# Kernel tuning notes

Hardware: AMD Instinct MI355X
Metric: run time of the kernel (lower is better)

## Reference

```python
import jax, jax.numpy as jnp
from jax import lax
import numpy as np

N_ASSETS = 128
BATCH = 2048
MAX_WEIGHT = 1.0
N_ITERS = 300      # projected-gradient iterations (unrolled solver)
N_BISECT = 40      # bisection steps for simplex-box projection
LR = 0.02
EPS = 1e-8


def project_capped_simplex(v, c):
    """Project rows of v onto {w : sum(w)=1, -c <= w <= c} via bisection on the
    shift tau in w = clip(v - tau, -c, c). sum is decreasing in tau."""
    lo = jnp.min(v, axis=-1, keepdims=True) - c - 1.0
    hi = jnp.max(v, axis=-1, keepdims=True) + c

    def body(carry, _):
        lo, hi = carry
        mid = 0.5 * (lo + hi)
        s = jnp.sum(jnp.clip(v - mid, -c, c), axis=-1, keepdims=True)
        too_big = s > 1.0
        return (jnp.where(too_big, mid, lo), jnp.where(too_big, hi, mid)), None

    (lo, hi), _ = lax.scan(body, (lo, hi), None, length=N_BISECT)
    tau = 0.5 * (lo + hi)
    return jnp.clip(v - tau, -c, c)


def solve_markowitz(rets, A, alpha_abs, max_weight):
    """maximize r.w - sqrt(w'Aw) - alpha*||w||_2  s.t. sum w = 1, |w| <= c,
    via projected gradient ascent (fixed iteration count, fully batched)."""
    B, n = rets.shape
    w0 = jnp.full((B, n), 1.0 / n, dtype=rets.dtype)
    a = alpha_abs[:, None]

    def step(w, _):
        Aw = jnp.einsum('bij,bj->bi', A, w)                       # (B,n)
        risk = jnp.sqrt(jnp.sum(w * Aw, axis=-1, keepdims=True) + EPS)
        nrm = jnp.sqrt(jnp.sum(w * w, axis=-1, keepdims=True) + EPS)
        g = rets - Aw / risk - a * (w / nrm)                      # gradient of objective
        w_new = project_capped_simplex(w + LR * g, max_weight)
        return w_new, None

    w, _ = lax.scan(step, w0, None, length=N_ITERS)
    return w


def setup_inputs() -> dict:
    key = jax.random.key(0)
    k1, k2, k3, k4 = jax.random.split(key, 4)
    rets = 0.05 * jax.random.normal(k1, (BATCH, N_ASSETS), dtype=jnp.float32)
    # PSD covariance: B B^T / n + jitter*I
    Bm = jax.random.normal(k2, (BATCH, N_ASSETS, N_ASSETS), dtype=jnp.float32)
    covmat = jnp.einsum('bik,bjk->bij', Bm, Bm) / N_ASSETS
    covmat = covmat + 1e-3 * jnp.eye(N_ASSETS, dtype=jnp.float32)
    gamma = jax.random.uniform(k3, (BATCH,), dtype=jnp.float32, minval=0.1, maxval=2.0)
    alpha = jax.random.normal(k4, (BATCH,), dtype=jnp.float32)
    return {"rets": rets, "covmat": covmat, "gamma": gamma, "alpha": alpha}


def reference(rets, covmat, gamma, alpha):
    alpha_abs = jnp.abs(alpha)
    A = gamma[:, None, None] * covmat   # gamma-adjusted covariance, as in forward
    return solve_markowitz(rets, A, alpha_abs, MAX_WEIGHT)
```

## Files before the change

### kernel.cpp

```cpp
#include <hip/hip_runtime.h>
#include <math.h>

#define NA      128
#define NBATCH  2048
#define NTHR    512
#define NIT     300
#define NBIS    40
#define LRC     0.02f
#define EPSC    1e-8f

template <int CTRL>
__device__ __forceinline__ float dpp_sum_step(float x) {
  int s = __builtin_amdgcn_update_dpp(0, __float_as_int(x), CTRL, 0xF, 0xF, true);
  return x + __int_as_float(s);
}
__device__ __forceinline__ float wave_sum64(float x) {
  x = dpp_sum_step<0x111>(x);
  x = dpp_sum_step<0x112>(x);
  x = dpp_sum_step<0x114>(x);
  x = dpp_sum_step<0x118>(x);
  x = dpp_sum_step<0x142>(x);
  x = dpp_sum_step<0x143>(x);
  return x;
}
template <int CTRL>
__device__ __forceinline__ float dpp_mov_self(float x) {
  int s = __builtin_amdgcn_update_dpp(__float_as_int(x), __float_as_int(x), CTRL, 0xF, 0xF, false);
  return __int_as_float(s);
}
__device__ __forceinline__ float wave_min64(float x) {
  x = fminf(x, dpp_mov_self<0x111>(x));
  x = fminf(x, dpp_mov_self<0x112>(x));
  x = fminf(x, dpp_mov_self<0x114>(x));
  x = fminf(x, dpp_mov_self<0x118>(x));
  x = fminf(x, dpp_mov_self<0x142>(x));
  x = fminf(x, dpp_mov_self<0x143>(x));
  return x;
}
__device__ __forceinline__ float wave_max64(float x) {
  x = fmaxf(x, dpp_mov_self<0x111>(x));
  x = fmaxf(x, dpp_mov_self<0x112>(x));
  x = fmaxf(x, dpp_mov_self<0x114>(x));
  x = fmaxf(x, dpp_mov_self<0x118>(x));
  x = fmaxf(x, dpp_mov_self<0x142>(x));
  x = fmaxf(x, dpp_mov_self<0x143>(x));
  return x;
}
__device__ __forceinline__ float bcast63(float x) {
  return __int_as_float(__builtin_amdgcn_readlane(__float_as_int(x), 63));
}
__device__ __forceinline__ float clip1(float x) {
  return __builtin_amdgcn_fmed3f(x, -1.0f, 1.0f);
}

__global__ __launch_bounds__(NTHR)
void markowitz_kernel(
    const float* __restrict__ rets,
    const float* __restrict__ covmat,
    const float* __restrict__ gamma,
    const float* __restrict__ alpha,
    float* __restrict__ out)
{
  const int b    = blockIdx.x;
  const int tid  = threadIdx.x;
  const int r    = tid & (NA - 1);
  const int q    = tid >> 7;
  const int lane = tid & 63;
  const int wv   = tid >> 6;
  const int chain_wv = b & 7;

  __shared__ __align__(16) float ws[NA];
  __shared__ __align__(16) float vs[NA];
  __shared__ __align__(16) float part[NTHR];
  __shared__ float pp[4];

  const float gm = gamma[b];
  const float4* Aq = reinterpret_cast<const float4*>(
      covmat + (size_t)b * NA * NA + (size_t)r * NA + (size_t)q * 32);
  float4 a[8];
#pragma unroll
  for (int k = 0; k < 8; ++k) {
    float4 t = Aq[k];
    a[k] = make_float4(t.x * gm, t.y * gm, t.z * gm, t.w * gm);
  }
  const float av = fabsf(alpha[b]);
  float r_c = 0.0f;
  if (tid < NA) { r_c = rets[b * NA + tid]; ws[tid] = 1.0f / NA; }
  __syncthreads();

#pragma unroll 1
  for (int it = 0; it < NIT; ++it) {
    const float4* w4 = reinterpret_cast<const float4*>(ws) + q * 8;
    float4 acc = make_float4(0.f, 0.f, 0.f, 0.f);
#pragma unroll
    for (int k = 0; k < 8; ++k) {
      float4 wk = w4[k];
      acc.x = fmaf(a[k].x, wk.x, acc.x);
      acc.y = fmaf(a[k].y, wk.y, acc.y);
      acc.z = fmaf(a[k].z, wk.z, acc.z);
      acc.w = fmaf(a[k].w, wk.w, acc.w);
    }
    part[tid] = (acc.x + acc.y) + (acc.z + acc.w);
    __syncthreads();

    float Aw = 0.f, w_c = 0.f, v_c = 0.f;
    if (tid < NA) {
      Aw  = (part[tid] + part[tid + NA]) + (part[tid + 2 * NA] + part[tid + 3 * NA]);
      w_c = ws[tid];
      float p1 = wave_sum64(w_c * Aw);
      float p2 = wave_sum64(w_c * w_c);
      if (lane == 63) { pp[wv * 2 + 0] = p1; pp[wv * 2 + 1] = p2; }
    }
    __syncthreads();

    if (tid < NA) {
      const float risk = sqrtf(pp[0] + pp[2] + EPSC);
      const float nrm  = sqrtf(pp[1] + pp[3] + EPSC);
      const float g    = r_c - Aw / risk - av * (w_c / nrm);
      v_c = w_c + LRC * g;
      vs[tid] = v_c;
    }
    __syncthreads();

    if (wv == chain_wv) {
      float v0 = vs[lane];
      float v1 = vs[lane + 64];
      float mn = bcast63(wave_min64(fminf(v0, v1)));
      float mx = bcast63(wave_max64(fmaxf(v0, v1)));
      float lo = mn - 2.0f;
      float hi = mx + 1.0f;
#pragma unroll 1
      for (int rr = 0; rr < NBIS; ++rr) {
        const float mid = 0.5f * (lo + hi);
        float s = wave_sum64(clip1(v0 - mid) + clip1(v1 - mid));
        const float st = bcast63(s);
        const bool big = st > 1.0f;
        lo = big ? mid : lo;
        hi = big ? hi : mid;
      }
      const float tau = 0.5f * (lo + hi);
      ws[lane]      = clip1(v0 - tau);
      ws[lane + 64] = clip1(v1 - tau);
    }
    __syncthreads();
  }

  if (tid < NA) out[b * NA + tid] = ws[tid];
}

extern "C" void kernel_launch(void* const* d_in, const int* in_sizes, int n_in,
                              void* d_out, int out_size, void* d_ws, size_t ws_size,
                              hipStream_t stream) {
  const float* rets   = (const float*)d_in[0];
  const float* covmat = (const float*)d_in[1];
  const float* gamma  = (const float*)d_in[2];
  const float* alpha  = (const float*)d_in[3];
  float* out = (float*)d_out;

  hipLaunchKernelGGL(markowitz_kernel, dim3(NBATCH), dim3(NTHR), 0, stream,
                     rets, covmat, gamma, alpha, out);
}
```

Before: 2.691 ms.

## Halve block size and stream covariance from memory each iteration instead of registers

Each block now runs 256 threads instead of 512, and every thread handles two 32-column segments of its covariance row. The gamma-scaled covariance is no longer held in registers for the whole solve; it is reloaded from global memory on every one of the 300 iterations and scaled by gamma inline. The aim is lower register pressure and higher occupancy, and the wave that runs the bisection is chosen with a different hash of the block index. The cost is about 64KB of covariance traffic per block per iteration, which likely exceeds cache capacity across all blocks and may make the kernel memory-bound.

Measured after the change: 3.261 ms. +21.1%, slower.

```diff
diff --git a/kernel.cpp b/kernel.cpp
--- a/kernel.cpp
+++ b/kernel.cpp
@@ -3,7 +3,7 @@
 
 #define NA      128
 #define NBATCH  2048
-#define NTHR    512
+#define NTHR    256
 #define NIT     300
 #define NBIS    40
 #define LRC     0.02f
@@ -64,25 +64,20 @@
   const int b    = blockIdx.x;
   const int tid  = threadIdx.x;
   const int r    = tid & (NA - 1);
-  const int q    = tid >> 7;
+  const int q0   = tid >> 7;
   const int lane = tid & 63;
   const int wv   = tid >> 6;
-  const int chain_wv = b & 7;
+  const int chain_wv = ((b >> 8) ^ b) & 3;
 
   __shared__ __align__(16) float ws[NA];
   __shared__ __align__(16) float vs[NA];
-  __shared__ __align__(16) float part[NTHR];
+  __shared__ __align__(16) float part[4 * NA];
   __shared__ float pp[4];
 
   const float gm = gamma[b];
-  const float4* Aq = reinterpret_cast<const float4*>(
-      covmat + (size_t)b * NA * NA + (size_t)r * NA + (size_t)q * 32);
-  float4 a[8];
-#pragma unroll
-  for (int k = 0; k < 8; ++k) {
-    float4 t = Aq[k];
-    a[k] = make_float4(t.x * gm, t.y * gm, t.z * gm, t.w * gm);
-  }
+  const float* Arow = covmat + (size_t)b * NA * NA + (size_t)r * NA + (size_t)q0 * 32;
+  const float4* Aq0 = reinterpret_cast<const float4*>(Arow);
+  const float4* Aq1 = reinterpret_cast<const float4*>(Arow + 64);
   const float av = fabsf(alpha[b]);
   float r_c = 0.0f;
   if (tid < NA) { r_c = rets[b * NA + tid]; ws[tid] = 1.0f / NA; }
@@ -90,20 +85,30 @@
 
 #pragma unroll 1
   for (int it = 0; it < NIT; ++it) {
-    const float4* w4 = reinterpret_cast<const float4*>(ws) + q * 8;
-    float4 acc = make_float4(0.f, 0.f, 0.f, 0.f);
+    const float4* w40 = reinterpret_cast<const float4*>(ws) + q0 * 8;
+    const float4* w41 = w40 + 16;
+    float4 acc0 = make_float4(0.f, 0.f, 0.f, 0.f);
+    float4 acc1 = make_float4(0.f, 0.f, 0.f, 0.f);
 #pragma unroll
     for (int k = 0; k < 8; ++k) {
-      float4 wk = w4[k];
-      acc.x = fmaf(a[k].x, wk.x, acc.x);
-      acc.y = fmaf(a[k].y, wk.y, acc.y);
-      acc.z = fmaf(a[k].z, wk.z, acc.z);
-      acc.w = fmaf(a[k].w, wk.w, acc.w);
+      float4 t0 = Aq0[k];
+      float4 wk0 = w40[k];
+      acc0.x = fmaf(t0.x * gm, wk0.x, acc0.x);
+      acc0.y = fmaf(t0.y * gm, wk0.y, acc0.y);
+      acc0.z = fmaf(t0.z * gm, wk0.z, acc0.z);
+      acc0.w = fmaf(t0.w * gm, wk0.w, acc0.w);
+      float4 t1 = Aq1[k];
+      float4 wk1 = w41[k];
+      acc1.x = fmaf(t1.x * gm, wk1.x, acc1.x);
+      acc1.y = fmaf(t1.y * gm, wk1.y, acc1.y);
+      acc1.z = fmaf(t1.z * gm, wk1.z, acc1.z);
+      acc1.w = fmaf(t1.w * gm, wk1.w, acc1.w);
     }
-    part[tid] = (acc.x + acc.y) + (acc.z + acc.w);
+    part[tid]       = (acc0.x + acc0.y) + (acc0.z + acc0.w);
+    part[tid + 256] = (acc1.x + acc1.y) + (acc1.z + acc1.w);
     __syncthreads();
 
-    float Aw = 0.f, w_c = 0.f, v_c = 0.f;
+    float Aw = 0.f, w_c = 0.f;
     if (tid < NA) {
       Aw  = (part[tid] + part[tid + NA]) + (part[tid + 2 * NA] + part[tid + 3 * NA]);
       w_c = ws[tid];
@@ -117,8 +122,7 @@
       const float risk = sqrtf(pp[0] + pp[2] + EPSC);
       const float nrm  = sqrtf(pp[1] + pp[3] + EPSC);
       const float g    = r_c - Aw / risk - av * (w_c / nrm);
-      v_c = w_c + LRC * g;
-      vs[tid] = v_c;
+      vs[tid] = w_c + LRC * g;
     }
     __syncthreads();
 
```

## Map one wave per batch element and batch bisection across eight elements

Applied to the files above, without the earlier changes.

Each block now handles eight batch elements, one wave apiece. Each lane computes two rows of A·w by streaming the covariance rows from global memory every iteration, instead of holding a register-resident slice of A. That removes the cross-wave partial-sum exchange and two barriers per iteration. The bisection for all eight elements runs in a single wave, using 8-lane groups and DPP/swizzle reductions, with eight values per lane. The trade-off is re-reading 64KB of A per element every iteration through cache, plus fewer blocks overall.

New measurement: 3.227 ms. 1.2x slower.

```diff
diff --git a/kernel.cpp b/kernel.cpp
--- a/kernel.cpp
+++ b/kernel.cpp
@@ -4,10 +4,12 @@
 #define NA      128
 #define NBATCH  2048
 #define NTHR    512
+#define NELB    8
 #define NIT     300
 #define NBIS    40
 #define LRC     0.02f
 #define EPSC    1e-8f
+
 
 template <int CTRL>
 __device__ __forceinline__ float dpp_sum_step(float x) {
@@ -23,31 +25,17 @@
   x = dpp_sum_step<0x143>(x);
   return x;
 }
+__device__ __forceinline__ float bcast63(float x) {
+  return __int_as_float(__builtin_amdgcn_readlane(__float_as_int(x), 63));
+}
 template <int CTRL>
-__device__ __forceinline__ float dpp_mov_self(float x) {
-  int s = __builtin_amdgcn_update_dpp(__float_as_int(x), __float_as_int(x), CTRL, 0xF, 0xF, false);
+__device__ __forceinline__ float dpp_qp(float x) {
+  int s = __builtin_amdgcn_update_dpp(0, __float_as_int(x), CTRL, 0xF, 0xF, true);
   return __int_as_float(s);
 }
-__device__ __forceinline__ float wave_min64(float x) {
-  x = fminf(x, dpp_mov_self<0x111>(x));
-  x = fminf(x, dpp_mov_self<0x112>(x));
-  x = fminf(x, dpp_mov_self<0x114>(x));
-  x = fminf(x, dpp_mov_self<0x118>(x));
-  x = fminf(x, dpp_mov_self<0x142>(x));
-  x = fminf(x, dpp_mov_self<0x143>(x));
-  return x;
-}
-__device__ __forceinline__ float wave_max64(float x) {
-  x = fmaxf(x, dpp_mov_self<0x111>(x));
-  x = fmaxf(x, dpp_mov_self<0x112>(x));
-  x = fmaxf(x, dpp_mov_self<0x114>(x));
-  x = fmaxf(x, dpp_mov_self<0x118>(x));
-  x = fmaxf(x, dpp_mov_self<0x142>(x));
-  x = fmaxf(x, dpp_mov_self<0x143>(x));
-  return x;
-}
-__device__ __forceinline__ float bcast63(float x) {
-  return __int_as_float(__builtin_amdgcn_readlane(__float_as_int(x), 63));
+__device__ __forceinline__ float swz_xor4(float x) {
+  int s = __builtin_amdgcn_ds_swizzle(__float_as_int(x), 0x101F);
+  return __int_as_float(s);
 }
 __device__ __forceinline__ float clip1(float x) {
   return __builtin_amdgcn_fmed3f(x, -1.0f, 1.0f);
@@ -63,89 +51,130 @@
 {
   const int b    = blockIdx.x;
   const int tid  = threadIdx.x;
-  const int r    = tid & (NA - 1);
-  const int q    = tid >> 7;
+  const int wv   = tid >> 6;
   const int lane = tid & 63;
-  const int wv   = tid >> 6;
-  const int chain_wv = b & 7;
+  const int e    = b * NELB + wv;
+  const int r0   = 2 * lane;
 
-  __shared__ __align__(16) float ws[NA];
-  __shared__ __align__(16) float vs[NA];
-  __shared__ __align__(16) float part[NTHR];
-  __shared__ float pp[4];
+  __shared__ __align__(16) float ws[NELB][NA];
+  __shared__ __align__(16) float vs[NELB][NA];
 
-  const float gm = gamma[b];
-  const float4* Aq = reinterpret_cast<const float4*>(
-      covmat + (size_t)b * NA * NA + (size_t)r * NA + (size_t)q * 32);
-  float4 a[8];
-#pragma unroll
-  for (int k = 0; k < 8; ++k) {
-    float4 t = Aq[k];
-    a[k] = make_float4(t.x * gm, t.y * gm, t.z * gm, t.w * gm);
-  }
-  const float av = fabsf(alpha[b]);
-  float r_c = 0.0f;
-  if (tid < NA) { r_c = rets[b * NA + tid]; ws[tid] = 1.0f / NA; }
+  const float gm = gamma[e];
+  const float av = fabsf(alpha[e]);
+  const float* A0 = covmat + (size_t)e * NA * NA + (size_t)r0 * NA;
+  const float2 rc = *reinterpret_cast<const float2*>(rets + (size_t)e * NA + r0);
+
+  *reinterpret_cast<float2*>(&ws[wv][r0]) = make_float2(1.0f / NA, 1.0f / NA);
   __syncthreads();
 
 #pragma unroll 1
   for (int it = 0; it < NIT; ++it) {
-    const float4* w4 = reinterpret_cast<const float4*>(ws) + q * 8;
-    float4 acc = make_float4(0.f, 0.f, 0.f, 0.f);
+    float qs0[4], qs1[4];
 #pragma unroll
-    for (int k = 0; k < 8; ++k) {
-      float4 wk = w4[k];
-      acc.x = fmaf(a[k].x, wk.x, acc.x);
-      acc.y = fmaf(a[k].y, wk.y, acc.y);
-      acc.z = fmaf(a[k].z, wk.z, acc.z);
-      acc.w = fmaf(a[k].w, wk.w, acc.w);
+    for (int q = 0; q < 4; ++q) {
+      const float4* a0 = reinterpret_cast<const float4*>(A0 + q * 32);
+      const float4* a1 = reinterpret_cast<const float4*>(A0 + NA + q * 32);
+      const float4* w4 = reinterpret_cast<const float4*>(ws[wv]) + q * 8;
+      float4 c0 = make_float4(0.f, 0.f, 0.f, 0.f);
+      float4 c1 = make_float4(0.f, 0.f, 0.f, 0.f);
+#pragma unroll
+      for (int k = 0; k < 8; ++k) {
+        float4 wk = w4[k];
+        float4 t0 = a0[k];
+        c0.x = fmaf(t0.x * gm, wk.x, c0.x);
+        c0.y = fmaf(t0.y * gm, wk.y, c0.y);
+        c0.z = fmaf(t0.z * gm, wk.z, c0.z);
+        c0.w = fmaf(t0.w * gm, wk.w, c0.w);
+        float4 t1 = a1[k];
+        c1.x = fmaf(t1.x * gm, wk.x, c1.x);
+        c1.y = fmaf(t1.y * gm, wk.y, c1.y);
+        c1.z = fmaf(t1.z * gm, wk.z, c1.z);
+        c1.w = fmaf(t1.w * gm, wk.w, c1.w);
+      }
+      qs0[q] = (c0.x + c0.y) + (c0.z + c0.w);
+      qs1[q] = (c1.x + c1.y) + (c1.z + c1.w);
     }
-    part[tid] = (acc.x + acc.y) + (acc.z + acc.w);
+    const float Aw0 = (qs0[0] + qs0[1]) + (qs0[2] + qs0[3]);
+    const float Aw1 = (qs1[0] + qs1[1]) + (qs1[2] + qs1[3]);
+
+    const float2 wp = *reinterpret_cast<const float2*>(&ws[wv][r0]);
+    float p0 = wp.x * Aw0, p1 = wp.y * Aw1;
+    asm volatile("" : "+v"(p0), "+v"(p1));
+    float u0 = wp.x * wp.x, u1 = wp.y * wp.y;
+    asm volatile("" : "+v"(u0), "+v"(u1));
+    const float sAw = bcast63(wave_sum64(p0 + p1));
+    const float sww = bcast63(wave_sum64(u0 + u1));
+
+    const float risk = sqrtf(sAw + EPSC);
+    const float nrm  = sqrtf(sww + EPSC);
+    const float g0 = rc.x - Aw0 / risk - av * (wp.x / nrm);
+    const float g1 = rc.y - Aw1 / risk - av * (wp.y / nrm);
+    const float v0 = wp.x + LRC * g0;
+    const float v1 = wp.y + LRC * g1;
+    *reinterpret_cast<float2*>(&vs[wv][r0]) = make_float2(v0, v1);
     __syncthreads();
 
-    float Aw = 0.f, w_c = 0.f, v_c = 0.f;
-    if (tid < NA) {
-      Aw  = (part[tid] + part[tid + NA]) + (part[tid + 2 * NA] + part[tid + 3 * NA]);
-      w_c = ws[tid];
-      float p1 = wave_sum64(w_c * Aw);
-      float p2 = wave_sum64(w_c * w_c);
-      if (lane == 63) { pp[wv * 2 + 0] = p1; pp[wv * 2 + 1] = p2; }
-    }
-    __syncthreads();
+    if (wv == 0) {
+      const int be = lane >> 3;
+      const int gg = lane & 7;
+      float4 la = *reinterpret_cast<const float4*>(&vs[be][8 * gg]);
+      float4 lb = *reinterpret_cast<const float4*>(&vs[be][8 * gg + 4]);
+      float4 ha = *reinterpret_cast<const float4*>(&vs[be][64 + 8 * gg]);
+      float4 hb = *reinterpret_cast<const float4*>(&vs[be][64 + 8 * gg + 4]);
+      const float vlo[8] = {la.x, la.y, la.z, la.w, lb.x, lb.y, lb.z, lb.w};
+      const float vhi[8] = {ha.x, ha.y, ha.z, ha.w, hb.x, hb.y, hb.z, hb.w};
 
-    if (tid < NA) {
-      const float risk = sqrtf(pp[0] + pp[2] + EPSC);
-      const float nrm  = sqrtf(pp[1] + pp[3] + EPSC);
-      const float g    = r_c - Aw / risk - av * (w_c / nrm);
-      v_c = w_c + LRC * g;
-      vs[tid] = v_c;
-    }
-    __syncthreads();
+      float mn = fminf(vlo[0], vhi[0]);
+      float mx = fmaxf(vlo[0], vhi[0]);
+#pragma unroll
+      for (int j = 1; j < 8; ++j) {
+        mn = fminf(mn, fminf(vlo[j], vhi[j]));
+        mx = fmaxf(mx, fmaxf(vlo[j], vhi[j]));
+      }
+      mn = fminf(mn, dpp_qp<0xB1>(mn));
+      mn = fminf(mn, dpp_qp<0x4E>(mn));
+      mn = fminf(mn, swz_xor4(mn));
+      mx = fmaxf(mx, dpp_qp<0xB1>(mx));
+      mx = fmaxf(mx, dpp_qp<0x4E>(mx));
+      mx = fmaxf(mx, swz_xor4(mx));
 
-    if (wv == chain_wv) {
-      float v0 = vs[lane];
-      float v1 = vs[lane + 64];
-      float mn = bcast63(wave_min64(fminf(v0, v1)));
-      float mx = bcast63(wave_max64(fmaxf(v0, v1)));
       float lo = mn - 2.0f;
       float hi = mx + 1.0f;
 #pragma unroll 1
       for (int rr = 0; rr < NBIS; ++rr) {
         const float mid = 0.5f * (lo + hi);
-        float s = wave_sum64(clip1(v0 - mid) + clip1(v1 - mid));
-        const float st = bcast63(s);
-        const bool big = st > 1.0f;
+        float t[8];
+#pragma unroll
+        for (int j = 0; j < 8; ++j)
+          t[j] = clip1(vlo[j] - mid) + clip1(vhi[j] - mid);
+        float s = ((t[0] + t[1]) + (t[2] + t[3])) + ((t[4] + t[5]) + (t[6] + t[7]));
+        s = s + dpp_qp<0xB1>(s);
+        s = s + dpp_qp<0x4E>(s);
+        s = s + swz_xor4(s);
+        const bool big = s > 1.0f;
         lo = big ? mid : lo;
         hi = big ? hi : mid;
       }
       const float tau = 0.5f * (lo + hi);
-      ws[lane]      = clip1(v0 - tau);
-      ws[lane + 64] = clip1(v1 - tau);
+      float4 o;
+      o.x = clip1(vlo[0] - tau); o.y = clip1(vlo[1] - tau);
+      o.z = clip1(vlo[2] - tau); o.w = clip1(vlo[3] - tau);
+      *reinterpret_cast<float4*>(&ws[be][8 * gg]) = o;
+      o.x = clip1(vlo[4] - tau); o.y = clip1(vlo[5] - tau);
+      o.z = clip1(vlo[6] - tau); o.w = clip1(vlo[7] - tau);
+      *reinterpret_cast<float4*>(&ws[be][8 * gg + 4]) = o;
+      o.x = clip1(vhi[0] - tau); o.y = clip1(vhi[1] - tau);
+      o.z = clip1(vhi[2] - tau); o.w = clip1(vhi[3] - tau);
+      *reinterpret_cast<float4*>(&ws[be][64 + 8 * gg]) = o;
+      o.x = clip1(vhi[4] - tau); o.y = clip1(vhi[5] - tau);
+      o.z = clip1(vhi[6] - tau); o.w = clip1(vhi[7] - tau);
+      *reinterpret_cast<float4*>(&ws[be][64 + 8 * gg + 4]) = o;
     }
     __syncthreads();
   }
 
-  if (tid < NA) out[b * NA + tid] = ws[tid];
+  *reinterpret_cast<float2*>(out + (size_t)e * NA + r0) =
+      make_float2(ws[wv][r0], ws[wv][r0 + 1]);
 }
 
 extern "C" void kernel_launch(void* const* d_in, const int* in_sizes, int n_in,
@@ -157,6 +186,6 @@
   const float* alpha  = (const float*)d_in[3];
   float* out = (float*)d_out;
 
-  hipLaunchKernelGGL(markowitz_kernel, dim3(NBATCH), dim3(NTHR), 0, stream,
+  hipLaunchKernelGGL(markowitz_kernel, dim3(NBATCH / NELB), dim3(NTHR), 0, stream,
                      rets, covmat, gamma, alpha, out);
 }
```
